# Kernel tuning notes

Measured on AMD Instinct MI355X. Metric: run time of the kernel, lower is better.

Reference implementation:

```python
import jax, jax.numpy as jnp
import numpy as np

# PCEN constants (from __init__ defaults)
ALPHA = 0.98
DELTA = 2.0
R = 0.5
S = 0.025
EPS = 1e-6


def setup_inputs() -> dict:
    key = jax.random.key(0)
    # mel spectrogram energies: [batch, mel_bins, time], nonnegative
    x = jax.random.uniform(key, (64, 128, 4096), dtype=jnp.float32)
    return {"x": x}


def _ema_smooth(x):
    # x: [B, C, T]. smooth[0] = x[0]; smooth[t] = (1-S)*smooth[t-1] + S*x[t]
    x_t = jnp.moveaxis(x, -1, 0)  # [T, B, C]
    init = x_t[0]

    def step(carry, xt):
        sm = (1.0 - S) * carry + S * xt
        return sm, sm

    _, rest = jax.lax.scan(step, init, x_t[1:])  # [T-1, B, C]
    smooth = jnp.concatenate([init[None], rest], axis=0)  # [T, B, C]
    return jnp.moveaxis(smooth, 0, -1)  # [B, C, T]


def reference(x):
    smooth = _ema_smooth(x)
    return (x / (smooth + EPS) ** ALPHA + DELTA) ** R - DELTA ** R
```

## Files before the change

kernel.cpp:

```cpp
#include <hip/hip_runtime.h>
#include <math.h>


#define T_LEN 4096
#define BLOCK 256
#define NSUB  16

constexpr double dpow(double b, int n) {
    double r = 1.0;
    for (int i = 0; i < n; ++i) r *= b;
    return r;
}

__global__ __launch_bounds__(BLOCK, 4) void pcen_kernel(const float* __restrict__ x,
                                                        float* __restrict__ out) {
    constexpr float A_COEF = 0.975f;
    constexpr float S_COEF = 0.025f;
    constexpr float ALPHA  = 0.98f;
    constexpr float EPS    = 1e-6f;
    constexpr float DELTA  = 2.0f;
    constexpr float SQRT_DELTA = 1.4142135623730951f;
    constexpr float CS0 = (float)dpow(0.975, 4);
    constexpr float CS1 = (float)dpow(0.975, 8);
    constexpr float CS2 = (float)dpow(0.975, 16);
    constexpr float CS3 = (float)dpow(0.975, 32);
    constexpr float CS4 = (float)dpow(0.975, 64);
    constexpr float CS5 = (float)dpow(0.975, 128);
    constexpr float A256 = (float)dpow(0.975, 256);
    constexpr float AP1 = (float)dpow(0.975, 1);
    constexpr float AP2 = (float)dpow(0.975, 2);
    constexpr float AP3 = (float)dpow(0.975, 3);
    constexpr float AP4 = (float)dpow(0.975, 4);

    const int tid  = threadIdx.x;
    const int lane = tid & 63;
    const int wid  = tid >> 6;
    const int row  = blockIdx.x * 4 + wid;

    const float* __restrict__ xr  = x   + (size_t)row * T_LEN;
    float* __restrict__       orr = out + (size_t)row * T_LEN;

    float a4l = 1.0f;
    a4l *= (lane & 1)  ? CS0 : 1.0f;
    a4l *= (lane & 2)  ? CS1 : 1.0f;
    a4l *= (lane & 4)  ? CS2 : 1.0f;
    a4l *= (lane & 8)  ? CS3 : 1.0f;
    a4l *= (lane & 16) ? CS4 : 1.0f;
    a4l *= (lane & 32) ? CS5 : 1.0f;

    float4 xq[NSUB];
#pragma unroll
    for (int s = 0; s < NSUB; ++s)
        xq[s] = *(const float4*)(xr + 256 * s + 4 * lane);

    float Bs[NSUB];
#pragma unroll
    for (int s = 0; s < NSUB; ++s) {
        float b = (s == 0 && lane == 0) ? xq[s].x : S_COEF * xq[s].x;
        b = fmaf(A_COEF, b, S_COEF * xq[s].y);
        b = fmaf(A_COEF, b, S_COEF * xq[s].z);
        b = fmaf(A_COEF, b, S_COEF * xq[s].w);
        float bu;
        bu = __shfl_up(b, 1);  if (lane >= 1)  b = fmaf(CS0, bu, b);
        bu = __shfl_up(b, 2);  if (lane >= 2)  b = fmaf(CS1, bu, b);
        bu = __shfl_up(b, 4);  if (lane >= 4)  b = fmaf(CS2, bu, b);
        bu = __shfl_up(b, 8);  if (lane >= 8)  b = fmaf(CS3, bu, b);
        bu = __shfl_up(b, 16); if (lane >= 16) b = fmaf(CS4, bu, b);
        bu = __shfl_up(b, 32); if (lane >= 32) b = fmaf(CS5, bu, b);
        Bs[s] = b;
    }

    float y = 0.0f;
#pragma unroll
    for (int s = 0; s < NSUB; ++s) {
        float bex = __shfl_up(Bs[s], 1);
        if (lane == 0) bex = 0.0f;
        float yl = fmaf(a4l, y, bex);

        float bi0 = (s == 0 && lane == 0) ? xq[s].x : S_COEF * xq[s].x;
        float bi1 = fmaf(A_COEF, bi0, S_COEF * xq[s].y);
        float bi2 = fmaf(A_COEF, bi1, S_COEF * xq[s].z);
        float bi3 = fmaf(A_COEF, bi2, S_COEF * xq[s].w);

        float sm0 = fmaf(AP1, yl, bi0);
        float sm1 = fmaf(AP2, yl, bi1);
        float sm2 = fmaf(AP3, yl, bi2);
        float sm3 = fmaf(AP4, yl, bi3);

        float4 o;
        {
            float p = __builtin_amdgcn_exp2f(-ALPHA * __builtin_amdgcn_logf(sm0 + EPS));
            o.x = __builtin_amdgcn_sqrtf(fmaf(xq[s].x, p, DELTA)) - SQRT_DELTA;
        }
        {
            float p = __builtin_amdgcn_exp2f(-ALPHA * __builtin_amdgcn_logf(sm1 + EPS));
            o.y = __builtin_amdgcn_sqrtf(fmaf(xq[s].y, p, DELTA)) - SQRT_DELTA;
        }
        {
            float p = __builtin_amdgcn_exp2f(-ALPHA * __builtin_amdgcn_logf(sm2 + EPS));
            o.z = __builtin_amdgcn_sqrtf(fmaf(xq[s].z, p, DELTA)) - SQRT_DELTA;
        }
        {
            float p = __builtin_amdgcn_exp2f(-ALPHA * __builtin_amdgcn_logf(sm3 + EPS));
            o.w = __builtin_amdgcn_sqrtf(fmaf(xq[s].w, p, DELTA)) - SQRT_DELTA;
        }
        *(float4*)(orr + 256 * s + 4 * lane) = o;

        y = fmaf(A256, y,
                 __uint_as_float(__builtin_amdgcn_readlane(__float_as_uint(Bs[s]), 63)));
    }
}

extern "C" void kernel_launch(void* const* d_in, const int* in_sizes, int n_in,
                              void* d_out, int out_size, void* d_ws, size_t ws_size,
                              hipStream_t stream) {
    const float* x = (const float*)d_in[0];
    float* out = (float*)d_out;
    const int rows = in_sizes[0] / T_LEN;
    pcen_kernel<<<rows / 4, BLOCK, 0, stream>>>(x, out);
}
```

Measured before the change: 232.4 us.

## Scan each row with a 1024-thread block using cross-wave shared-memory prefix

```diff
diff --git a/kernel.cpp b/kernel.cpp
--- a/kernel.cpp
+++ b/kernel.cpp
@@ -3,8 +3,9 @@
 
 
 #define T_LEN 4096
-#define BLOCK 256
-#define NSUB  16
+#define BLOCK 1024
+#define PER   4
+#define NWAVE (BLOCK / 64)
 
 constexpr double dpow(double b, int n) {
     double r = 1.0;
@@ -12,8 +13,8 @@
     return r;
 }
 
-__global__ __launch_bounds__(BLOCK, 4) void pcen_kernel(const float* __restrict__ x,
-                                                        float* __restrict__ out) {
+__global__ __launch_bounds__(BLOCK) void pcen_kernel(const float* __restrict__ x,
+                                                     float* __restrict__ out) {
     constexpr float A_COEF = 0.975f;
     constexpr float S_COEF = 0.025f;
     constexpr float ALPHA  = 0.98f;
@@ -30,15 +31,43 @@
     constexpr float AP1 = (float)dpow(0.975, 1);
     constexpr float AP2 = (float)dpow(0.975, 2);
     constexpr float AP3 = (float)dpow(0.975, 3);
-    constexpr float AP4 = (float)dpow(0.975, 4);
+
+    const int row = blockIdx.x;
+    const float* __restrict__ xr  = x   + (size_t)row * T_LEN;
+    float* __restrict__       orr = out + (size_t)row * T_LEN;
 
     const int tid  = threadIdx.x;
     const int lane = tid & 63;
     const int wid  = tid >> 6;
-    const int row  = blockIdx.x * 4 + wid;
+    const int base = tid * PER;
 
-    const float* __restrict__ xr  = x   + (size_t)row * T_LEN;
-    float* __restrict__       orr = out + (size_t)row * T_LEN;
+    float4 v = *(const float4*)(xr + base);
+
+    float b0 = (tid == 0) ? v.x : S_COEF * v.x;
+    float b1 = fmaf(A_COEF, b0, S_COEF * v.y);
+    float b2 = fmaf(A_COEF, b1, S_COEF * v.z);
+    float b3 = fmaf(A_COEF, b2, S_COEF * v.w);
+
+    float B = b3;
+    float bu;
+    bu = __shfl_up(B, 1);  if (lane >= 1)  B = fmaf(CS0, bu, B);
+    bu = __shfl_up(B, 2);  if (lane >= 2)  B = fmaf(CS1, bu, B);
+    bu = __shfl_up(B, 4);  if (lane >= 4)  B = fmaf(CS2, bu, B);
+    bu = __shfl_up(B, 8);  if (lane >= 8)  B = fmaf(CS3, bu, B);
+    bu = __shfl_up(B, 16); if (lane >= 16) B = fmaf(CS4, bu, B);
+    bu = __shfl_up(B, 32); if (lane >= 32) B = fmaf(CS5, bu, B);
+
+    __shared__ float wB[NWAVE];
+    if (lane == 63) wB[wid] = B;
+    __syncthreads();
+
+    float Bex = __shfl_up(B, 1);
+    if (lane == 0) Bex = 0.0f;
+
+    float WB = 0.0f;
+    for (int w = 0; w < wid; ++w) {
+        WB = fmaf(A256, WB, wB[w]);
+    }
 
     float a4l = 1.0f;
     a4l *= (lane & 1)  ? CS0 : 1.0f;
@@ -48,67 +77,31 @@
     a4l *= (lane & 16) ? CS4 : 1.0f;
     a4l *= (lane & 32) ? CS5 : 1.0f;
 
-    float4 xq[NSUB];
-#pragma unroll
-    for (int s = 0; s < NSUB; ++s)
-        xq[s] = *(const float4*)(xr + 256 * s + 4 * lane);
+    float y_in = fmaf(a4l, WB, Bex);
 
-    float Bs[NSUB];
-#pragma unroll
-    for (int s = 0; s < NSUB; ++s) {
-        float b = (s == 0 && lane == 0) ? xq[s].x : S_COEF * xq[s].x;
-        b = fmaf(A_COEF, b, S_COEF * xq[s].y);
-        b = fmaf(A_COEF, b, S_COEF * xq[s].z);
-        b = fmaf(A_COEF, b, S_COEF * xq[s].w);
-        float bu;
-        bu = __shfl_up(b, 1);  if (lane >= 1)  b = fmaf(CS0, bu, b);
-        bu = __shfl_up(b, 2);  if (lane >= 2)  b = fmaf(CS1, bu, b);
-        bu = __shfl_up(b, 4);  if (lane >= 4)  b = fmaf(CS2, bu, b);
-        bu = __shfl_up(b, 8);  if (lane >= 8)  b = fmaf(CS3, bu, b);
-        bu = __shfl_up(b, 16); if (lane >= 16) b = fmaf(CS4, bu, b);
-        bu = __shfl_up(b, 32); if (lane >= 32) b = fmaf(CS5, bu, b);
-        Bs[s] = b;
+    float sm0 = fmaf(AP1, y_in, b0);
+    float sm1 = fmaf(AP2, y_in, b1);
+    float sm2 = fmaf(AP3, y_in, b2);
+    float sm3 = fmaf(CS0, y_in, b3);
+
+    float4 o;
+    {
+        float p = __builtin_amdgcn_exp2f(-ALPHA * __builtin_amdgcn_logf(sm0 + EPS));
+        o.x = __builtin_amdgcn_sqrtf(fmaf(v.x, p, DELTA)) - SQRT_DELTA;
     }
-
-    float y = 0.0f;
-#pragma unroll
-    for (int s = 0; s < NSUB; ++s) {
-        float bex = __shfl_up(Bs[s], 1);
-        if (lane == 0) bex = 0.0f;
-        float yl = fmaf(a4l, y, bex);
-
-        float bi0 = (s == 0 && lane == 0) ? xq[s].x : S_COEF * xq[s].x;
-        float bi1 = fmaf(A_COEF, bi0, S_COEF * xq[s].y);
-        float bi2 = fmaf(A_COEF, bi1, S_COEF * xq[s].z);
-        float bi3 = fmaf(A_COEF, bi2, S_COEF * xq[s].w);
-
-        float sm0 = fmaf(AP1, yl, bi0);
-        float sm1 = fmaf(AP2, yl, bi1);
-        float sm2 = fmaf(AP3, yl, bi2);
-        float sm3 = fmaf(AP4, yl, bi3);
-
-        float4 o;
-        {
-            float p = __builtin_amdgcn_exp2f(-ALPHA * __builtin_amdgcn_logf(sm0 + EPS));
-            o.x = __builtin_amdgcn_sqrtf(fmaf(xq[s].x, p, DELTA)) - SQRT_DELTA;
-        }
-        {
-            float p = __builtin_amdgcn_exp2f(-ALPHA * __builtin_amdgcn_logf(sm1 + EPS));
-            o.y = __builtin_amdgcn_sqrtf(fmaf(xq[s].y, p, DELTA)) - SQRT_DELTA;
-        }
-        {
-            float p = __builtin_amdgcn_exp2f(-ALPHA * __builtin_amdgcn_logf(sm2 + EPS));
-            o.z = __builtin_amdgcn_sqrtf(fmaf(xq[s].z, p, DELTA)) - SQRT_DELTA;
-        }
-        {
-            float p = __builtin_amdgcn_exp2f(-ALPHA * __builtin_amdgcn_logf(sm3 + EPS));
-            o.w = __builtin_amdgcn_sqrtf(fmaf(xq[s].w, p, DELTA)) - SQRT_DELTA;
-        }
-        *(float4*)(orr + 256 * s + 4 * lane) = o;
-
-        y = fmaf(A256, y,
-                 __uint_as_float(__builtin_amdgcn_readlane(__float_as_uint(Bs[s]), 63)));
+    {
+        float p = __builtin_amdgcn_exp2f(-ALPHA * __builtin_amdgcn_logf(sm1 + EPS));
+        o.y = __builtin_amdgcn_sqrtf(fmaf(v.y, p, DELTA)) - SQRT_DELTA;
     }
+    {
+        float p = __builtin_amdgcn_exp2f(-ALPHA * __builtin_amdgcn_logf(sm2 + EPS));
+        o.z = __builtin_amdgcn_sqrtf(fmaf(v.z, p, DELTA)) - SQRT_DELTA;
+    }
+    {
+        float p = __builtin_amdgcn_exp2f(-ALPHA * __builtin_amdgcn_logf(sm3 + EPS));
+        o.w = __builtin_amdgcn_sqrtf(fmaf(v.w, p, DELTA)) - SQRT_DELTA;
+    }
+    *(float4*)(orr + base) = o;
 }
 
 extern "C" void kernel_launch(void* const* d_in, const int* in_sizes, int n_in,
@@ -117,5 +110,5 @@
     const float* x = (const float*)d_in[0];
     float* out = (float*)d_out;
     const int rows = in_sizes[0] / T_LEN;
-    pcen_kernel<<<rows / 4, BLOCK, 0, stream>>>(x, out);
+    pcen_kernel<<<rows, BLOCK, 0, stream>>>(x, out);
 }
```

Result: faster. 222.6 us (-4.2%).
